# Optimization experiments

Hardware: AMD Instinct MI355X
Metric: run time of the kernel (lower is better)

## Reference

```python
import jax, jax.numpy as jnp
import numpy as np

B, N = 8, 8192
S_ATTN, S_NONE = 128, 384          # npoint = (npoint_all=512, npoint_none_attn=384) -> npoint_attn=128
S = S_ATTN + S_NONE
NSAMPLE = 64
RADIUS = 0.4
D_FEAT = 64
MLP = [64, 64, 128]
IN_CH = 3 + D_FEAT


def fps(pts, K):
    # pytorch3d.sample_farthest_points, start index 0, full lengths. pts: [B,N,3]
    B_, N_, _ = pts.shape
    def body(carry, _):
        min_d2, last = carry
        lp = jnp.take_along_axis(pts, last[:, None, None], axis=1)      # [B,1,3]
        d2 = jnp.sum((pts - lp) ** 2, -1)                               # [B,N]
        min_d2 = jnp.minimum(min_d2, d2)
        nxt = jnp.argmax(min_d2, -1).astype(jnp.int32)
        return (min_d2, nxt), last
    init = (jnp.full((B_, N_), jnp.float32(1e10)), jnp.zeros((B_,), jnp.int32))
    _, idxs = jax.lax.scan(body, init, None, length=K)
    idxs = idxs.T                                                       # [B,K]
    sampled = jnp.take_along_axis(pts, idxs[..., None], axis=1)         # [B,K,3]
    return sampled, idxs


def ball_query(query, pts, K, radius):
    # pytorch3d.ball_query: first K points with d2 < r^2 in index order; idx pad=-1, nn pad=0.
    d2 = jnp.sum((query[:, :, None, :] - pts[:, None, :, :]) ** 2, -1)  # [B,S,N]
    mask = d2 < radius * radius
    order = jnp.cumsum(mask.astype(jnp.int32), -1) - 1
    slot = jnp.where(mask & (order < K), order, K)                      # overflow -> dump slot K
    n_ids = jnp.broadcast_to(jnp.arange(pts.shape[1], dtype=jnp.int32), slot.shape)
    def scatter_row(slot_row, ids_row):
        return jnp.full((K + 1,), -1, jnp.int32).at[slot_row].set(ids_row)[:K]
    idx = jax.vmap(jax.vmap(scatter_row))(slot, n_ids)                  # [B,S,K]
    valid = idx >= 0
    gathered = jax.vmap(lambda p, i: p[i])(pts, jnp.where(valid, idx, 0))  # [B,S,K,3]
    nn = jnp.where(valid[..., None], gathered, 0.0)
    return idx, nn


def _forward(xyz, points, attention, ws, bs):
    xyz_t = xyz.transpose(0, 2, 1)            # [B,N,3]
    pts_t = points.transpose(0, 2, 1)         # [B,N,D]
    attn_t = attention.transpose(0, 2, 1)     # [B,N,1]

    attn_xyz = attn_t * xyz_t
    none_xyz = (1.0 - attn_t) * xyz_t
    new_attn_xyz, idx_a = fps(attn_xyz, S_ATTN)
    new_none_xyz, idx_n = fps(none_xyz, S_NONE)
    new_xyz = jnp.concatenate([new_attn_xyz, new_none_xyz], axis=1)     # [B,S,3]
    fps_idx = jnp.concatenate([idx_a, idx_n], axis=1)                   # [B,S]
    new_attention = jnp.take_along_axis(attn_t, fps_idx[..., None], axis=1)  # [B,S,1]

    idx, grouped_xyz = ball_query(new_xyz, xyz_t, NSAMPLE, RADIUS)
    grouped_norm = grouped_xyz - new_xyz[:, :, None, :]                 # [B,S,K,3]
    gather_idx = jnp.where(idx < 0, N - 1, idx)   # torch index -1 wraps to last point
    grouped_pts = jax.vmap(lambda p, i: p[i])(pts_t, gather_idx)        # [B,S,K,D]
    feat = jnp.concatenate([grouped_norm, grouped_pts], -1)             # [B,S,K,3+D]

    x = feat.transpose(0, 3, 2, 1)                                      # [B,C,K,S]
    for w, b in zip(ws, bs):                                            # 1x1 Conv2d + ReLU
        x = jax.nn.relu(jnp.einsum('oc,bcks->boks', w, x) + b[None, :, None, None])
    new_points = jnp.max(x, axis=2)                                     # MaxPool over nsample -> [B,C',S]
    return new_xyz.transpose(0, 2, 1), new_points, new_attention.transpose(0, 2, 1)


def setup_inputs() -> dict:
    key = jax.random.key(0)
    ks = jax.random.split(key, 8)
    xyz = jax.random.normal(ks[0], (B, 3, N), jnp.float32)
    points = jax.random.normal(ks[1], (B, D_FEAT, N), jnp.float32)
    attention = jnp.round(jax.random.uniform(ks[2], (B, 1, N), jnp.float32))  # 0/1 mask
    inp = {'xyz': xyz, 'points': points, 'attention': attention}
    last = IN_CH
    for i, oc in enumerate(MLP):
        inp[f'w{i}'] = jax.random.normal(ks[3 + i], (oc, last), jnp.float32) / np.float32(np.sqrt(last))
        inp[f'b{i}'] = jnp.zeros((oc,), jnp.float32)
        last = oc
    return inp


def reference(xyz, points, attention, w0, b0, w1, b1, w2, b2):
    return _forward(xyz, points, attention, (w0, w1, w2), (b0, b1, b2))
```

## Files before the change

### kernel.cpp

```cpp
#include <hip/hip_runtime.h>
#include <cstdint>
#include <cstddef>

#define NB 8
#define NPTS 8192
#define S_TOT 512
#define NSAMP 64
#define DFEAT 64
#define INCH 67
#define SLOTS 17
#define CCAP (SLOTS * 256)

typedef __attribute__((ext_vector_type(8))) short v8s;
typedef __attribute__((ext_vector_type(4))) short v4s;
typedef __attribute__((ext_vector_type(4))) float v4f;

__device__ __forceinline__ float d2_exact(float ax, float ay, float az,
                                          float bx, float by, float bz) {
    float dx = __fsub_rn(ax, bx);
    float dy = __fsub_rn(ay, by);
    float dz = __fsub_rn(az, bz);
    return __fadd_rn(__fadd_rn(__fmul_rn(dx, dx), __fmul_rn(dy, dy)), __fmul_rn(dz, dz));
}

__device__ __forceinline__ unsigned short f2b(float f) {
    unsigned u = __float_as_uint(f);
    return (unsigned short)((u + 0x7fffu + ((u >> 16) & 1u)) >> 16);
}

template <int CTRL>
__device__ __forceinline__ unsigned long long dpp_max_u64(unsigned long long k) {
    int lo = (int)(unsigned)(k & 0xffffffffull);
    int hi = (int)(unsigned)(k >> 32);
    int slo = __builtin_amdgcn_update_dpp(lo, lo, CTRL, 0xf, 0xf, false);
    int shi = __builtin_amdgcn_update_dpp(hi, hi, CTRL, 0xf, 0xf, false);
    unsigned long long o = ((unsigned long long)(unsigned)shi << 32) | (unsigned)slo;
    return (o > k) ? o : k;
}

__global__ __launch_bounds__(1024) void fps_compact(
    const float* __restrict__ xyz, const float* __restrict__ attn,
    float4* __restrict__ cxyz, int* __restrict__ hdr)
{
    int blk = blockIdx.x;
    int b = blk >> 1, grp = blk & 1;
    const float* xb = xyz + (size_t)b * 3 * NPTS;
    const float* ab = attn + (size_t)b * NPTS;
    float4* c4 = cxyz + (size_t)blk * CCAP;

    int tid = threadIdx.x, lane = tid & 63, wid = tid >> 6;
    int n0 = tid * 8;

    __shared__ int s_repmin;
    __shared__ int s_ws[16];
    if (tid == 0) s_repmin = NPTS;
    __syncthreads();

    float av[8];
    *(float4*)&av[0] = *(const float4*)(ab + n0);
    *(float4*)&av[4] = *(const float4*)(ab + n0 + 4);
    int cnt = 0, mymin = NPTS;
    bool keep[8];
#pragma unroll
    for (int j = 0; j < 8; j++) {
        keep[j] = grp ? (av[j] == 0.0f) : (av[j] != 0.0f);
        cnt += keep[j] ? 1 : 0;
        if (!keep[j] && n0 + j < mymin) mymin = n0 + j;
    }
    if (mymin < NPTS) atomicMin(&s_repmin, mymin);

    int incl = cnt;
#pragma unroll
    for (int off = 1; off <= 32; off <<= 1) {
        int t = __shfl_up(incl, off);
        if (lane >= off) incl += t;
    }
    if (lane == 63) s_ws[wid] = incl;
    __syncthreads();
    int woff = 0, tot = 0;
#pragma unroll
    for (int w = 0; w < 16; w++) { if (w < wid) woff += s_ws[w]; tot += s_ws[w]; }
    int pos = woff + incl - cnt;
    int rm = s_repmin;
    int rm_eff = (rm < NPTS) ? rm : 0x7fffffff;

    float xv[8], yv[8], zv[8];
    *(float4*)&xv[0] = *(const float4*)(xb + n0);
    *(float4*)&xv[4] = *(const float4*)(xb + n0 + 4);
    *(float4*)&yv[0] = *(const float4*)(xb + NPTS + n0);
    *(float4*)&yv[4] = *(const float4*)(xb + NPTS + n0 + 4);
    *(float4*)&zv[0] = *(const float4*)(xb + 2 * NPTS + n0);
    *(float4*)&zv[4] = *(const float4*)(xb + 2 * NPTS + n0 + 4);
#pragma unroll
    for (int j = 0; j < 8; j++) {
        if (keep[j]) {
            int fin = pos + ((n0 + j > rm_eff) ? 1 : 0);
            if (fin < CCAP)
                c4[fin] = make_float4(xv[j], yv[j], zv[j], 0.0f);
            pos++;
        }
    }
    if (tid == 0) {
        int M = tot;
        if (rm < NPTS) {
            if (rm < CCAP)
                c4[rm] = make_float4(__fmul_rn(0.0f, xb[rm]),
                                     __fmul_rn(0.0f, xb[NPTS + rm]),
                                     __fmul_rn(0.0f, xb[2 * NPTS + rm]), 0.0f);
            M++;
        }
        hdr[blk * 2] = M;
        hdr[blk * 2 + 1] = (rm < NPTS) ? rm : -1;
    }
}

__global__ __launch_bounds__(256, 1) void fps_iter(
    const float* __restrict__ attn,
    const float4* __restrict__ cxyz,
    const int* __restrict__ hdr,
    float* __restrict__ out0, float* __restrict__ out2)
{
    int blk = blockIdx.x;
    int b = blk >> 1, grp = blk & 1;
    int K = grp ? 384 : 128;
    int soff = grp ? 128 : 0;
    int M = hdr[blk * 2];
    int repslot = hdr[blk * 2 + 1];
    if (M > CCAP) return;
    int tid = threadIdx.x, lane = tid & 63, wid = tid >> 6;

    const float4* cb = cxyz + (size_t)blk * CCAP;
    __shared__ float4 sc[CCAP];
    __shared__ float4 s_obuf[384];
    __shared__ __align__(16) unsigned long long s_red[2][4];

    float px[SLOTS], py[SLOTS], pz[SLOTS], md[SLOTS];
#pragma unroll
    for (int i = 0; i < SLOTS; i++) {
        int sl = i * 256 + tid;
        bool v = sl < M;
        float4 c = v ? cb[sl] : make_float4(0.f, 0.f, 0.f, 0.f);
        px[i] = c.x; py[i] = c.y; pz[i] = c.z;
        sc[sl] = c;
        md[i] = v ? 1e10f : -1.0f;
    }
    float4 c0 = cb[0];
    float lx = c0.x, ly = c0.y, lz = c0.z;
    float a_last = attn[(size_t)b * NPTS];
    float kept_a = grp ? 0.0f : 1.0f;
    float rep_a  = grp ? 1.0f : 0.0f;

    for (int k = 0; k < K; k++) {
        if (tid == 0) s_obuf[k] = make_float4(lx, ly, lz, a_last);
        if (k == K - 1) break;

        float bv = -1.0f; int bslot = 0x7fffffff;
#pragma unroll
        for (int i = 0; i < SLOTS; i++) {
            float d2 = d2_exact(px[i], py[i], pz[i], lx, ly, lz);
            md[i] = fminf(md[i], d2);
            int sl = i * 256 + tid;
            bool w = (md[i] > bv) || ((md[i] == bv) && (sl < bslot));
            bv = w ? md[i] : bv;
            bslot = w ? sl : bslot;
        }
        unsigned long long key = (bv >= 0.0f)
            ? (((unsigned long long)__float_as_uint(bv) << 32) | (unsigned)(~bslot))
            : 0ull;
        key = dpp_max_u64<0x111>(key);
        key = dpp_max_u64<0x112>(key);
        key = dpp_max_u64<0x114>(key);
        key = dpp_max_u64<0x118>(key);
        key = dpp_max_u64<0x142>(key);
        key = dpp_max_u64<0x143>(key);
        int buf = k & 1;
        if (lane == 63) s_red[buf][wid] = key;
        __syncthreads();

        const unsigned long long* rp = s_red[buf];
        unsigned long long k0 = rp[0], k1 = rp[1], k2 = rp[2], k3 = rp[3];
        unsigned long long m01 = (k0 > k1) ? k0 : k1;
        unsigned long long m23 = (k2 > k3) ? k2 : k3;
        unsigned long long g = (m01 > m23) ? m01 : m23;
        int wslot = (int)(~(unsigned)g);
        float4 wc = sc[wslot];
        lx = wc.x; ly = wc.y; lz = wc.z;
        a_last = (wslot == repslot) ? rep_a : kept_a;
    }
    __syncthreads();
    for (int k2i = tid; k2i < K; k2i += 256) {
        float4 o = s_obuf[k2i];
        int sg = soff + k2i;
        out0[(size_t)b * 3 * S_TOT + sg] = o.x;
        out0[(size_t)b * 3 * S_TOT + S_TOT + sg] = o.y;
        out0[(size_t)b * 3 * S_TOT + 2 * S_TOT + sg] = o.z;
        out2[(size_t)b * S_TOT + sg] = o.w;
    }
}

__global__ __launch_bounds__(1024, 1) void fps_kernel(
    const float* __restrict__ xyz, const float* __restrict__ attn,
    const int* __restrict__ hdr,
    float* __restrict__ out0, float* __restrict__ out2)
{
    int blk = blockIdx.x;
    if (hdr != nullptr && hdr[blk * 2] <= CCAP) return;
    int b = blk >> 1, grp = blk & 1;
    int K = grp ? 384 : 128;
    int soff = grp ? 128 : 0;
    int tid = threadIdx.x, lane = tid & 63, wid = tid >> 6;
    const float* xb = xyz + (size_t)b * 3 * NPTS;
    const float* ab = attn + (size_t)b * NPTS;

    float px[8], py[8], pz[8], md[8];
#pragma unroll
    for (int i = 0; i < 8; i++) {
        int n = tid + i * 1024;
        float a = ab[n];
        float f = grp ? __fsub_rn(1.0f, a) : a;
        px[i] = __fmul_rn(f, xb[n]);
        py[i] = __fmul_rn(f, xb[NPTS + n]);
        pz[i] = __fmul_rn(f, xb[2 * NPTS + n]);
        md[i] = 1e10f;
    }
    __shared__ unsigned long long s_red[2][16];
    float a_last = ab[0];
    float f0 = grp ? __fsub_rn(1.0f, a_last) : a_last;
    float lx = __fmul_rn(f0, xb[0]);
    float ly = __fmul_rn(f0, xb[NPTS]);
    float lz = __fmul_rn(f0, xb[2 * NPTS]);

    for (int k = 0; k < K; k++) {
        if (tid == 0) {
            int sg = soff + k;
            out0[(size_t)b * 3 * S_TOT + sg] = lx;
            out0[(size_t)b * 3 * S_TOT + S_TOT + sg] = ly;
            out0[(size_t)b * 3 * S_TOT + 2 * S_TOT + sg] = lz;
            out2[(size_t)b * S_TOT + sg] = a_last;
        }
        if (k == K - 1) break;
        float bv = -1.0f; int bi = 0;
#pragma unroll
        for (int i = 0; i < 8; i++) {
            float d2 = d2_exact(px[i], py[i], pz[i], lx, ly, lz);
            md[i] = fminf(md[i], d2);
            if (md[i] > bv) { bv = md[i]; bi = tid + i * 1024; }
        }
        unsigned long long best =
            ((unsigned long long)__float_as_uint(bv) << 32) | (unsigned)(~bi);
#pragma unroll
        for (int off = 32; off >= 1; off >>= 1) {
            unsigned long long o = __shfl_down(best, off);
            best = (o > best) ? o : best;
        }
        if (lane == 0) s_red[k & 1][wid] = best;
        __syncthreads();
        unsigned long long r = (lane < 16) ? s_red[k & 1][lane] : 0ull;
#pragma unroll
        for (int off = 8; off >= 1; off >>= 1) {
            unsigned long long o = __shfl_down(r, off);
            r = (o > r) ? o : r;
        }
        r = __shfl(r, 0);
        int n = (int)(~(unsigned)r);
        a_last = ab[n];
        float fl = grp ? __fsub_rn(1.0f, a_last) : a_last;
        lx = __fmul_rn(fl, xb[n]);
        ly = __fmul_rn(fl, xb[NPTS + n]);
        lz = __fmul_rn(fl, xb[2 * NPTS + n]);
    }
}

__global__ __launch_bounds__(256) void prep_kernel(
    const float* __restrict__ pts, unsigned short* __restrict__ ptsTh,
    const float* __restrict__ w0, const float* __restrict__ w1,
    const float* __restrict__ w2, unsigned short* __restrict__ wp)
{
    int blk = blockIdx.x;
    if (blk < 1024) {
        __shared__ float t[64][65];
        int b = blk >> 7;
        int n0 = (blk & 127) * 64;
        int tx = threadIdx.x & 63, ty = threadIdx.x >> 6;
        for (int c = ty; c < 64; c += 4)
            t[c][tx] = pts[((size_t)b * DFEAT + c) * NPTS + n0 + tx];
        __syncthreads();
        for (int r = ty; r < 64; r += 4)
            ptsTh[((size_t)b * NPTS + n0 + r) * DFEAT + tx] = f2b(t[tx][r]);
    } else if (threadIdx.x < 64) {
        int t = blk - 1024, l = threadIdx.x;
        int kq = (l >> 4) * 8, n16 = l & 15;
        unsigned short o[8];
#pragma unroll
        for (int j = 0; j < 8; j++) {
            float v;
            if (t < 12) {
                int kt = t >> 2, nt = t & 3;
                int k = kt * 32 + kq + j, n = nt * 16 + n16;
                v = (k < 64) ? w0[n * INCH + 3 + k] : (k < 67 ? w0[n * INCH + (k - 64)] : 0.0f);
            } else if (t < 20) {
                int tt = t - 12, kt = tt >> 2, nt = tt & 3;
                v = w1[(nt * 16 + n16) * 64 + kt * 32 + kq + j];
            } else {
                int tt = t - 20, kt = tt >> 3, nt = tt & 7;
                v = w2[(nt * 16 + n16) * 64 + kt * 32 + kq + j];
            }
            o[j] = f2b(v);
        }
        *(v8s*)&wp[(size_t)t * 512 + l * 8] = *(v8s*)o;
    }
}

__global__ __launch_bounds__(64, 2) void ball_mlp_mfma(
    const float* __restrict__ xyz,
    const unsigned short* __restrict__ ptsTh,
    const unsigned short* __restrict__ wp,
    const float* __restrict__ b0, const float* __restrict__ b1,
    const float* __restrict__ b2,
    const float* __restrict__ out0,
    float* __restrict__ out1)
{
    const float R2 = (float)(0.4 * 0.4);
    int q = blockIdx.x;
    int b = q >> 9;
    int sg = q & 511;
    int lane = threadIdx.x;
    int col = lane & 15, quad = lane >> 4, kq = quad * 8;

    const float* xb = xyz + (size_t)b * 3 * NPTS;
    float qx = out0[(size_t)b * 3 * S_TOT + sg];
    float qy = out0[(size_t)b * 3 * S_TOT + S_TOT + sg];
    float qz = out0[(size_t)b * 3 * S_TOT + 2 * S_TOT + sg];

    __shared__ int s_idx[NSAMP];
    __shared__ __align__(16) short sBuf[64 * 104];
    unsigned long long* s_mask = (unsigned long long*)sBuf;

#pragma unroll 8
    for (int j = 0; j < 128; j++) {
        int n = j * 64 + lane;
        float d2 = d2_exact(qx, qy, qz, xb[n], xb[NPTS + n], xb[2 * NPTS + n]);
        unsigned long long m = __ballot(d2 < R2);
        if (lane == 0) s_mask[j] = m;
    }

    unsigned long long m0 = s_mask[lane];
    unsigned long long m1 = s_mask[64 + lane];
    int c0 = (int)__popcll(m0), c1 = (int)__popcll(m1);
    int i0 = c0;
#pragma unroll
    for (int off = 1; off <= 32; off <<= 1) {
        int t = __shfl_up(i0, off);
        if (lane >= off) i0 += t;
    }
    int T0 = __shfl(i0, 63);
    int i1 = c1;
#pragma unroll
    for (int off = 1; off <= 32; off <<= 1) {
        int t = __shfl_up(i1, off);
        if (lane >= off) i1 += t;
    }
    int total = T0 + __shfl(i1, 63);
    int p0 = i0 - c0;
    int p1 = T0 + i1 - c1;

    {
        int base = p0, org = lane * 64;
        while (m0 && base < NSAMP) {
            int bp = __ffsll((long long)m0) - 1;
            s_idx[base++] = org + bp;
            m0 &= m0 - 1;
        }
        base = p1; org = (64 + lane) * 64;
        while (m1 && base < NSAMP) {
            int bp = __ffsll((long long)m1) - 1;
            s_idx[base++] = org + bp;
            m1 &= m1 - 1;
        }
    }
    int cnt = (total > NSAMP) ? NSAMP : total;

    int nb = (lane < cnt) ? s_idx[lane] : -1;
    float nx_ = 0.f, ny_ = 0.f, nz_ = 0.f;
    if (nb >= 0) { nx_ = xb[nb]; ny_ = xb[NPTS + nb]; nz_ = xb[2 * NPTS + nb]; }
    float fx = nx_ - qx, fy = ny_ - qy, fz = nz_ - qz;
    int row = (nb < 0) ? (NPTS - 1) : nb;

    {
        const unsigned short* ph = ptsTh + ((size_t)b * NPTS + row) * DFEAT;
        short* xr = &sBuf[lane * 104];
#pragma unroll
        for (int i = 0; i < 8; i++)
            *(v8s*)(xr + i * 8) = *(const v8s*)(ph + i * 8);
#pragma unroll
        for (int i = 0; i < 5; i++)
            *(v8s*)(xr + 64 + i * 8) = (v8s)0;
        v4s xyzp;
        xyzp[0] = (short)f2b(fx); xyzp[1] = (short)f2b(fy);
        xyzp[2] = (short)f2b(fz); xyzp[3] = 0;
        *(v4s*)(xr + 64) = xyzp;
    }

    const v8s* wpv = (const v8s*)wp;

    v4f acc[4][4];
#pragma unroll
    for (int nt = 0; nt < 4; nt++) {
        float bb = b0[nt * 16 + col];
#pragma unroll
        for (int mt = 0; mt < 4; mt++) acc[mt][nt] = (v4f){bb, bb, bb, bb};
    }
#pragma unroll
    for (int kt = 0; kt < 3; kt++) {
        v8s bf[4];
#pragma unroll
        for (int nt = 0; nt < 4; nt++) bf[nt] = wpv[(kt * 4 + nt) * 64 + lane];
#pragma unroll
        for (int mt = 0; mt < 4; mt++) {
            v8s a = *(const v8s*)&sBuf[(mt * 16 + col) * 104 + kt * 32 + kq];
#pragma unroll
            for (int nt = 0; nt < 4; nt++)
                acc[mt][nt] = __builtin_amdgcn_mfma_f32_16x16x32_bf16(a, bf[nt], acc[mt][nt], 0, 0, 0);
        }
    }
#pragma unroll
    for (int mt = 0; mt < 4; mt++)
#pragma unroll
        for (int nt = 0; nt < 4; nt++)
#pragma unroll
            for (int r = 0; r < 4; r++)
                sBuf[(mt * 16 + quad * 4 + r) * 72 + nt * 16 + col] =
                    (short)f2b(fmaxf(acc[mt][nt][r], 0.0f));

#pragma unroll
    for (int nt = 0; nt < 4; nt++) {
        float bb = b1[nt * 16 + col];
#pragma unroll
        for (int mt = 0; mt < 4; mt++) acc[mt][nt] = (v4f){bb, bb, bb, bb};
    }
#pragma unroll
    for (int kt = 0; kt < 2; kt++) {
        v8s bf[4];
#pragma unroll
        for (int nt = 0; nt < 4; nt++) bf[nt] = wpv[(12 + kt * 4 + nt) * 64 + lane];
#pragma unroll
        for (int mt = 0; mt < 4; mt++) {
            v8s a = *(const v8s*)&sBuf[(mt * 16 + col) * 72 + kt * 32 + kq];
#pragma unroll
            for (int nt = 0; nt < 4; nt++)
                acc[mt][nt] = __builtin_amdgcn_mfma_f32_16x16x32_bf16(a, bf[nt], acc[mt][nt], 0, 0, 0);
        }
    }
#pragma unroll
    for (int mt = 0; mt < 4; mt++)
#pragma unroll
        for (int nt = 0; nt < 4; nt++)
#pragma unroll
            for (int r = 0; r < 4; r++)
                sBuf[(mt * 16 + quad * 4 + r) * 72 + nt * 16 + col] =
                    (short)f2b(fmaxf(acc[mt][nt][r], 0.0f));

#pragma unroll
    for (int p = 0; p < 2; p++) {
#pragma unroll
        for (int nt = 0; nt < 4; nt++) {
            float bb = b2[(p * 4 + nt) * 16 + col];
#pragma unroll
            for (int mt = 0; mt < 4; mt++) acc[mt][nt] = (v4f){bb, bb, bb, bb};
        }
#pragma unroll
        for (int kt = 0; kt < 2; kt++) {
            v8s bf[4];
#pragma unroll
            for (int nt = 0; nt < 4; nt++)
                bf[nt] = wpv[(20 + kt * 8 + p * 4 + nt) * 64 + lane];
#pragma unroll
            for (int mt = 0; mt < 4; mt++) {
                v8s a = *(const v8s*)&sBuf[(mt * 16 + col) * 72 + kt * 32 + kq];
#pragma unroll
                for (int nt = 0; nt < 4; nt++)
                    acc[mt][nt] = __builtin_amdgcn_mfma_f32_16x16x32_bf16(a, bf[nt], acc[mt][nt], 0, 0, 0);
            }
        }
#pragma unroll
        for (int nt = 0; nt < 4; nt++) {
            float v = 0.0f;
#pragma unroll
            for (int mt = 0; mt < 4; mt++)
#pragma unroll
                for (int r = 0; r < 4; r++)
                    v = fmaxf(v, acc[mt][nt][r]);
            v = fmaxf(v, __shfl_xor(v, 16));
            v = fmaxf(v, __shfl_xor(v, 32));
            if (lane < 16)
                out1[((size_t)(b * 128 + (p * 4 + nt) * 16 + lane)) * S_TOT + sg] = v;
        }
    }
}

__global__ __launch_bounds__(64, 1) void ball_mlp_fb(
    const float* __restrict__ xyz, const float* __restrict__ pts,
    const float* __restrict__ w0, const float* __restrict__ b0,
    const float* __restrict__ w1, const float* __restrict__ b1,
    const float* __restrict__ w2, const float* __restrict__ b2,
    const float* __restrict__ out0, float* __restrict__ out1)
{
    const float R2 = (float)(0.4 * 0.4);
    int q = blockIdx.x;
    int b = q >> 9, sg = q & 511, lane = threadIdx.x;
    const float* xb = xyz + (size_t)b * 3 * NPTS;
    float qx = out0[(size_t)b * 3 * S_TOT + sg];
    float qy = out0[(size_t)b * 3 * S_TOT + S_TOT + sg];
    float qz = out0[(size_t)b * 3 * S_TOT + 2 * S_TOT + sg];

    __shared__ int s_idx[NSAMP];
    __shared__ float s_h[32 * 64];
    int cnt = 0;
    for (int base = 0; base < NPTS; base += 64) {
        int n = base + lane;
        float d2 = d2_exact(qx, qy, qz, xb[n], xb[NPTS + n], xb[2 * NPTS + n]);
        bool flag = d2 < R2;
        unsigned long long m = __ballot(flag);
        int pos = cnt + (int)__popcll(m & ((1ull << lane) - 1ull));
        if (flag && pos < NSAMP) s_idx[pos] = n;
        cnt += (int)__popcll(m);
    }
    if (cnt > NSAMP) cnt = NSAMP;
    int nb = (lane < cnt) ? s_idx[lane] : -1;
    float nx_ = 0.f, ny_ = 0.f, nz_ = 0.f;
    if (nb >= 0) { nx_ = xb[nb]; ny_ = xb[NPTS + nb]; nz_ = xb[2 * NPTS + nb]; }
    float fx = nx_ - qx, fy = ny_ - qy, fz = nz_ - qz;
    int row = (nb < 0) ? (NPTS - 1) : nb;

    float h1[64];
#pragma unroll
    for (int o = 0; o < 64; o++) {
        float a = __builtin_fmaf(w0[o * INCH + 0], fx, b0[o]);
        a = __builtin_fmaf(w0[o * INCH + 1], fy, a);
        h1[o] = __builtin_fmaf(w0[o * INCH + 2], fz, a);
    }
    const float* pb = pts + (size_t)b * DFEAT * NPTS + row;
#pragma unroll 1
    for (int c = 0; c < 64; c++) {
        float f = pb[(size_t)c * NPTS];
#pragma unroll
        for (int o = 0; o < 64; o++)
            h1[o] = __builtin_fmaf(w0[o * INCH + 3 + c], f, h1[o]);
    }
#pragma unroll
    for (int c = 0; c < 32; c++) s_h[c * 64 + lane] = fmaxf(h1[c], 0.0f);
    float h1h[32];
#pragma unroll
    for (int c = 0; c < 32; c++) h1h[c] = fmaxf(h1[32 + c], 0.0f);

    float h2[64];
#pragma unroll
    for (int o = 0; o < 64; o++) h2[o] = b1[o];
#pragma unroll 1
    for (int c = 0; c < 32; c++) {
        float hc = s_h[c * 64 + lane];
#pragma unroll
        for (int o = 0; o < 64; o++)
            h2[o] = __builtin_fmaf(w1[o * 64 + c], hc, h2[o]);
    }
#pragma unroll
    for (int c = 0; c < 32; c++) s_h[c * 64 + lane] = h1h[c];
#pragma unroll 1
    for (int c = 0; c < 32; c++) {
        float hc = s_h[c * 64 + lane];
#pragma unroll
        for (int o = 0; o < 64; o++)
            h2[o] = __builtin_fmaf(w1[o * 64 + (32 + c)], hc, h2[o]);
    }
#pragma unroll
    for (int o = 0; o < 64; o++) h2[o] = fmaxf(h2[o], 0.0f);

#pragma unroll 2
    for (int o = 0; o < 128; o++) {
        const float* wr = w2 + o * 64;
        float acc = b2[o];
#pragma unroll
        for (int c = 0; c < 64; c++) acc = __builtin_fmaf(wr[c], h2[c], acc);
        acc = fmaxf(acc, 0.0f);
#pragma unroll
        for (int off = 32; off >= 1; off >>= 1)
            acc = fmaxf(acc, __shfl_down(acc, off));
        if (lane == 0) out1[((size_t)(b * 128 + o)) * S_TOT + sg] = acc;
    }
}

extern "C" void kernel_launch(void* const* d_in, const int* in_sizes, int n_in,
                              void* d_out, int out_size, void* d_ws, size_t ws_size,
                              hipStream_t stream) {
    const float* xyz  = (const float*)d_in[0];
    const float* pts  = (const float*)d_in[1];
    const float* attn = (const float*)d_in[2];
    const float* w0 = (const float*)d_in[3];
    const float* b0 = (const float*)d_in[4];
    const float* w1 = (const float*)d_in[5];
    const float* b1 = (const float*)d_in[6];
    const float* w2 = (const float*)d_in[7];
    const float* b2 = (const float*)d_in[8];

    float* out0 = (float*)d_out;
    float* out1 = out0 + (size_t)NB * 3 * S_TOT;
    float* out2 = out1 + (size_t)NB * 128 * S_TOT;

    unsigned short* wp    = (unsigned short*)d_ws;
    unsigned short* ptsTh = (unsigned short*)((char*)d_ws + 36864);
    float4*         cxyz  = (float4*)((char*)d_ws + 36864 + 8388608);
    int*            hdr   = (int*)((char*)cxyz + (size_t)16 * CCAP * 16);
    const size_t need = 36864 + 8388608 + (size_t)16 * CCAP * 16 + 128;

    if (ws_size >= need) {
        fps_compact<<<16, 1024, 0, stream>>>(xyz, attn, cxyz, hdr);
        fps_iter<<<16, 256, 0, stream>>>(attn, cxyz, hdr, out0, out2);
        fps_kernel<<<16, 1024, 0, stream>>>(xyz, attn, hdr, out0, out2);
        prep_kernel<<<1060, 256, 0, stream>>>(pts, ptsTh, w0, w1, w2, wp);
        ball_mlp_mfma<<<NB * S_TOT, 64, 0, stream>>>(xyz, ptsTh, wp, b0, b1, b2,
                                                     out0, out1);
    } else {
        fps_kernel<<<16, 1024, 0, stream>>>(xyz, attn, nullptr, out0, out2);
        ball_mlp_fb<<<NB * S_TOT, 64, 0, stream>>>(xyz, pts, w0, b0, w1, b1,
                                                   w2, b2, out0, out1);
    }
}
```

Measured before the change: 643.0 us.

## Merge prep into compaction kernel and replace FPS barrier with stamped spin

The weight/feature bf16 prep work is folded into the FPS compaction launch as extra blocks (1024-thread blocks now). This removes one launch and lets the prep run alongside compaction. In the FPS iteration loop, the per-step __syncthreads is replaced by per-wave key+stamp slots in LDS that every thread spins on, and sampled points are written straight to global memory by thread 0 instead of being buffered. This cuts barrier cost in a serial loop of up to 384 steps. The spin-wait leans on volatile LDS ordering with no fence between the key and stamp writes, which risks subtle races.

New measurement: 751.8 us. 16.9% more time.

```diff
diff --git a/kernel.cpp b/kernel.cpp
--- a/kernel.cpp
+++ b/kernel.cpp
@@ -38,79 +38,118 @@
     return (o > k) ? o : k;
 }
 
-__global__ __launch_bounds__(1024) void fps_compact(
+__global__ __launch_bounds__(1024) void front_kernel(
     const float* __restrict__ xyz, const float* __restrict__ attn,
-    float4* __restrict__ cxyz, int* __restrict__ hdr)
+    float4* __restrict__ cxyz, int* __restrict__ hdr,
+    const float* __restrict__ pts, unsigned short* __restrict__ ptsTh,
+    const float* __restrict__ w0, const float* __restrict__ w1,
+    const float* __restrict__ w2, unsigned short* __restrict__ wp)
 {
     int blk = blockIdx.x;
-    int b = blk >> 1, grp = blk & 1;
-    const float* xb = xyz + (size_t)b * 3 * NPTS;
-    const float* ab = attn + (size_t)b * NPTS;
-    float4* c4 = cxyz + (size_t)blk * CCAP;
-
-    int tid = threadIdx.x, lane = tid & 63, wid = tid >> 6;
-    int n0 = tid * 8;
-
-    __shared__ int s_repmin;
-    __shared__ int s_ws[16];
-    if (tid == 0) s_repmin = NPTS;
-    __syncthreads();
-
-    float av[8];
-    *(float4*)&av[0] = *(const float4*)(ab + n0);
-    *(float4*)&av[4] = *(const float4*)(ab + n0 + 4);
-    int cnt = 0, mymin = NPTS;
-    bool keep[8];
-#pragma unroll
-    for (int j = 0; j < 8; j++) {
-        keep[j] = grp ? (av[j] == 0.0f) : (av[j] != 0.0f);
-        cnt += keep[j] ? 1 : 0;
-        if (!keep[j] && n0 + j < mymin) mymin = n0 + j;
-    }
-    if (mymin < NPTS) atomicMin(&s_repmin, mymin);
-
-    int incl = cnt;
-#pragma unroll
-    for (int off = 1; off <= 32; off <<= 1) {
-        int t = __shfl_up(incl, off);
-        if (lane >= off) incl += t;
-    }
-    if (lane == 63) s_ws[wid] = incl;
-    __syncthreads();
-    int woff = 0, tot = 0;
-#pragma unroll
-    for (int w = 0; w < 16; w++) { if (w < wid) woff += s_ws[w]; tot += s_ws[w]; }
-    int pos = woff + incl - cnt;
-    int rm = s_repmin;
-    int rm_eff = (rm < NPTS) ? rm : 0x7fffffff;
-
-    float xv[8], yv[8], zv[8];
-    *(float4*)&xv[0] = *(const float4*)(xb + n0);
-    *(float4*)&xv[4] = *(const float4*)(xb + n0 + 4);
-    *(float4*)&yv[0] = *(const float4*)(xb + NPTS + n0);
-    *(float4*)&yv[4] = *(const float4*)(xb + NPTS + n0 + 4);
-    *(float4*)&zv[0] = *(const float4*)(xb + 2 * NPTS + n0);
-    *(float4*)&zv[4] = *(const float4*)(xb + 2 * NPTS + n0 + 4);
-#pragma unroll
-    for (int j = 0; j < 8; j++) {
-        if (keep[j]) {
-            int fin = pos + ((n0 + j > rm_eff) ? 1 : 0);
-            if (fin < CCAP)
-                c4[fin] = make_float4(xv[j], yv[j], zv[j], 0.0f);
-            pos++;
-        }
-    }
-    if (tid == 0) {
-        int M = tot;
-        if (rm < NPTS) {
-            if (rm < CCAP)
-                c4[rm] = make_float4(__fmul_rn(0.0f, xb[rm]),
-                                     __fmul_rn(0.0f, xb[NPTS + rm]),
-                                     __fmul_rn(0.0f, xb[2 * NPTS + rm]), 0.0f);
-            M++;
-        }
-        hdr[blk * 2] = M;
-        hdr[blk * 2 + 1] = (rm < NPTS) ? rm : -1;
+    int tid = threadIdx.x;
+
+    if (blk < 16) {
+        int b = blk >> 1, grp = blk & 1;
+        const float* xb = xyz + (size_t)b * 3 * NPTS;
+        const float* ab = attn + (size_t)b * NPTS;
+        float4* c4 = cxyz + (size_t)blk * CCAP;
+
+        int lane = tid & 63, wid = tid >> 6;
+        int n0 = tid * 8;
+
+        __shared__ int s_repmin;
+        __shared__ int s_ws[16];
+        if (tid == 0) s_repmin = NPTS;
+        __syncthreads();
+
+        float av[8];
+        *(float4*)&av[0] = *(const float4*)(ab + n0);
+        *(float4*)&av[4] = *(const float4*)(ab + n0 + 4);
+        int cnt = 0, mymin = NPTS;
+        bool keep[8];
+#pragma unroll
+        for (int j = 0; j < 8; j++) {
+            keep[j] = grp ? (av[j] == 0.0f) : (av[j] != 0.0f);
+            cnt += keep[j] ? 1 : 0;
+            if (!keep[j] && n0 + j < mymin) mymin = n0 + j;
+        }
+        if (mymin < NPTS) atomicMin(&s_repmin, mymin);
+
+        int incl = cnt;
+#pragma unroll
+        for (int off = 1; off <= 32; off <<= 1) {
+            int t = __shfl_up(incl, off);
+            if (lane >= off) incl += t;
+        }
+        if (lane == 63) s_ws[wid] = incl;
+        __syncthreads();
+        int woff = 0, tot = 0;
+#pragma unroll
+        for (int w = 0; w < 16; w++) { if (w < wid) woff += s_ws[w]; tot += s_ws[w]; }
+        int pos = woff + incl - cnt;
+        int rm = s_repmin;
+        int rm_eff = (rm < NPTS) ? rm : 0x7fffffff;
+
+        float xv[8], yv[8], zv[8];
+        *(float4*)&xv[0] = *(const float4*)(xb + n0);
+        *(float4*)&xv[4] = *(const float4*)(xb + n0 + 4);
+        *(float4*)&yv[0] = *(const float4*)(xb + NPTS + n0);
+        *(float4*)&yv[4] = *(const float4*)(xb + NPTS + n0 + 4);
+        *(float4*)&zv[0] = *(const float4*)(xb + 2 * NPTS + n0);
+        *(float4*)&zv[4] = *(const float4*)(xb + 2 * NPTS + n0 + 4);
+#pragma unroll
+        for (int j = 0; j < 8; j++) {
+            if (keep[j]) {
+                int fin = pos + ((n0 + j > rm_eff) ? 1 : 0);
+                if (fin < CCAP)
+                    c4[fin] = make_float4(xv[j], yv[j], zv[j], 0.0f);
+                pos++;
+            }
+        }
+        if (tid == 0) {
+            int M = tot;
+            if (rm < NPTS) {
+                if (rm < CCAP)
+                    c4[rm] = make_float4(__fmul_rn(0.0f, xb[rm]),
+                                         __fmul_rn(0.0f, xb[NPTS + rm]),
+                                         __fmul_rn(0.0f, xb[2 * NPTS + rm]), 0.0f);
+                M++;
+            }
+            hdr[blk * 2] = M;
+            hdr[blk * 2 + 1] = (rm < NPTS) ? rm : -1;
+        }
+    } else if (blk < 16 + 1024) {
+        __shared__ float t[64][65];
+        int blk2 = blk - 16;
+        int b = blk2 >> 7;
+        int n0 = (blk2 & 127) * 64;
+        int tx = tid & 63, ty = tid >> 6;
+        for (int c = ty; c < 64; c += 16)
+            t[c][tx] = pts[((size_t)b * DFEAT + c) * NPTS + n0 + tx];
+        __syncthreads();
+        for (int r = ty; r < 64; r += 16)
+            ptsTh[((size_t)b * NPTS + n0 + r) * DFEAT + tx] = f2b(t[tx][r]);
+    } else if (tid < 64) {
+        int t = blk - (16 + 1024), l = tid;
+        int kq = (l >> 4) * 8, n16 = l & 15;
+        unsigned short o[8];
+#pragma unroll
+        for (int j = 0; j < 8; j++) {
+            float v;
+            if (t < 12) {
+                int kt = t >> 2, nt = t & 3;
+                int k = kt * 32 + kq + j, n = nt * 16 + n16;
+                v = (k < 64) ? w0[n * INCH + 3 + k] : (k < 67 ? w0[n * INCH + (k - 64)] : 0.0f);
+            } else if (t < 20) {
+                int tt = t - 12, kt = tt >> 2, nt = tt & 3;
+                v = w1[(nt * 16 + n16) * 64 + kt * 32 + kq + j];
+            } else {
+                int tt = t - 20, kt = tt >> 3, nt = tt & 7;
+                v = w2[(nt * 16 + n16) * 64 + kt * 32 + kq + j];
+            }
+            o[j] = f2b(v);
+        }
+        *(v8s*)&wp[(size_t)t * 512 + l * 8] = *(v8s*)o;
     }
 }
 
@@ -131,8 +170,10 @@
 
     const float4* cb = cxyz + (size_t)blk * CCAP;
     __shared__ float4 sc[CCAP];
-    __shared__ float4 s_obuf[384];
-    __shared__ __align__(16) unsigned long long s_red[2][4];
+    __shared__ __align__(16) unsigned long long s_key[2][4];
+    __shared__ int s_stamp[2][4];
+
+    if (tid < 8) s_stamp[tid >> 2][tid & 3] = -1;
 
     float px[SLOTS], py[SLOTS], pz[SLOTS], md[SLOTS];
 #pragma unroll
@@ -144,6 +185,8 @@
         sc[sl] = c;
         md[i] = v ? 1e10f : -1.0f;
     }
+    __syncthreads();
+
     float4 c0 = cb[0];
     float lx = c0.x, ly = c0.y, lz = c0.z;
     float a_last = attn[(size_t)b * NPTS];
@@ -151,7 +194,13 @@
     float rep_a  = grp ? 1.0f : 0.0f;
 
     for (int k = 0; k < K; k++) {
-        if (tid == 0) s_obuf[k] = make_float4(lx, ly, lz, a_last);
+        if (tid == 0) {
+            int sg = soff + k;
+            out0[(size_t)b * 3 * S_TOT + sg] = lx;
+            out0[(size_t)b * 3 * S_TOT + S_TOT + sg] = ly;
+            out0[(size_t)b * 3 * S_TOT + 2 * S_TOT + sg] = lz;
+            out2[(size_t)b * S_TOT + sg] = a_last;
+        }
         if (k == K - 1) break;
 
         float bv = -1.0f; int bslot = 0x7fffffff;
@@ -174,27 +223,30 @@
         key = dpp_max_u64<0x142>(key);
         key = dpp_max_u64<0x143>(key);
         int buf = k & 1;
-        if (lane == 63) s_red[buf][wid] = key;
-        __syncthreads();
-
-        const unsigned long long* rp = s_red[buf];
-        unsigned long long k0 = rp[0], k1 = rp[1], k2 = rp[2], k3 = rp[3];
-        unsigned long long m01 = (k0 > k1) ? k0 : k1;
-        unsigned long long m23 = (k2 > k3) ? k2 : k3;
+        if (lane == 63) {
+            volatile unsigned long long* kp = &s_key[buf][wid];
+            volatile int* sp = &s_stamp[buf][wid];
+            *kp = key;
+            *sp = k;
+        }
+
+        {
+            volatile int* sp = &s_stamp[buf][0];
+            for (;;) {
+                int s0 = sp[0], s1 = sp[1], s2 = sp[2], s3 = sp[3];
+                if (s0 == k && s1 == k && s2 == k && s3 == k) break;
+            }
+        }
+        volatile unsigned long long* kp = &s_key[buf][0];
+        unsigned long long kk0 = kp[0], kk1 = kp[1], kk2 = kp[2], kk3 = kp[3];
+
+        unsigned long long m01 = (kk0 > kk1) ? kk0 : kk1;
+        unsigned long long m23 = (kk2 > kk3) ? kk2 : kk3;
         unsigned long long g = (m01 > m23) ? m01 : m23;
         int wslot = (int)(~(unsigned)g);
         float4 wc = sc[wslot];
         lx = wc.x; ly = wc.y; lz = wc.z;
         a_last = (wslot == repslot) ? rep_a : kept_a;
-    }
-    __syncthreads();
-    for (int k2i = tid; k2i < K; k2i += 256) {
-        float4 o = s_obuf[k2i];
-        int sg = soff + k2i;
-        out0[(size_t)b * 3 * S_TOT + sg] = o.x;
-        out0[(size_t)b * 3 * S_TOT + S_TOT + sg] = o.y;
-        out0[(size_t)b * 3 * S_TOT + 2 * S_TOT + sg] = o.z;
-        out2[(size_t)b * S_TOT + sg] = o.w;
     }
 }
 
@@ -268,46 +320,6 @@
         lx = __fmul_rn(fl, xb[n]);
         ly = __fmul_rn(fl, xb[NPTS + n]);
         lz = __fmul_rn(fl, xb[2 * NPTS + n]);
-    }
-}
-
-__global__ __launch_bounds__(256) void prep_kernel(
-    const float* __restrict__ pts, unsigned short* __restrict__ ptsTh,
-    const float* __restrict__ w0, const float* __restrict__ w1,
-    const float* __restrict__ w2, unsigned short* __restrict__ wp)
-{
-    int blk = blockIdx.x;
-    if (blk < 1024) {
-        __shared__ float t[64][65];
-        int b = blk >> 7;
-        int n0 = (blk & 127) * 64;
-        int tx = threadIdx.x & 63, ty = threadIdx.x >> 6;
-        for (int c = ty; c < 64; c += 4)
-            t[c][tx] = pts[((size_t)b * DFEAT + c) * NPTS + n0 + tx];
-        __syncthreads();
-        for (int r = ty; r < 64; r += 4)
-            ptsTh[((size_t)b * NPTS + n0 + r) * DFEAT + tx] = f2b(t[tx][r]);
-    } else if (threadIdx.x < 64) {
-        int t = blk - 1024, l = threadIdx.x;
-        int kq = (l >> 4) * 8, n16 = l & 15;
-        unsigned short o[8];
-#pragma unroll
-        for (int j = 0; j < 8; j++) {
-            float v;
-            if (t < 12) {
-                int kt = t >> 2, nt = t & 3;
-                int k = kt * 32 + kq + j, n = nt * 16 + n16;
-                v = (k < 64) ? w0[n * INCH + 3 + k] : (k < 67 ? w0[n * INCH + (k - 64)] : 0.0f);
-            } else if (t < 20) {
-                int tt = t - 12, kt = tt >> 2, nt = tt & 3;
-                v = w1[(nt * 16 + n16) * 64 + kt * 32 + kq + j];
-            } else {
-                int tt = t - 20, kt = tt >> 3, nt = tt & 7;
-                v = w2[(nt * 16 + n16) * 64 + kt * 32 + kq + j];
-            }
-            o[j] = f2b(v);
-        }
-        *(v8s*)&wp[(size_t)t * 512 + l * 8] = *(v8s*)o;
     }
 }
 
@@ -613,10 +625,10 @@
     const size_t need = 36864 + 8388608 + (size_t)16 * CCAP * 16 + 128;
 
     if (ws_size >= need) {
-        fps_compact<<<16, 1024, 0, stream>>>(xyz, attn, cxyz, hdr);
+        front_kernel<<<16 + 1024 + 36, 1024, 0, stream>>>(
+            xyz, attn, cxyz, hdr, pts, ptsTh, w0, w1, w2, wp);
         fps_iter<<<16, 256, 0, stream>>>(attn, cxyz, hdr, out0, out2);
         fps_kernel<<<16, 1024, 0, stream>>>(xyz, attn, hdr, out0, out2);
-        prep_kernel<<<1060, 256, 0, stream>>>(pts, ptsTh, w0, w1, w2, wp);
         ball_mlp_mfma<<<NB * S_TOT, 64, 0, stream>>>(xyz, ptsTh, wp, b0, b1, b2,
                                                      out0, out1);
     } else {
```
